# Optimization experiments

Hardware: AMD Instinct MI355X
Metric: run time of the kernel (lower is better)

The kernel has to match this reference:

```python
import jax, jax.numpy as jnp
import numpy as np

LN_EPS = 1e-5  # torch nn.LayerNorm default

def _layer_norm(x, w, b):
    m = jnp.mean(x, axis=-1, keepdims=True)
    v = jnp.mean(jnp.square(x - m), axis=-1, keepdims=True)
    return (x - m) * jax.lax.rsqrt(v + LN_EPS) * w + b

def setup_inputs() -> dict:
    R, N, D, A = 8, 8192, 2048, 128
    init_scale = 0.01
    key = jax.random.key(0)
    k0, k1, k2 = jax.random.split(key, 3)
    x = jax.random.normal(k0, (N, D), jnp.float32)
    ln_w = jnp.ones((R, D), jnp.float32)              # per-router input LayerNorm weight
    ln_b = jnp.zeros((R, D), jnp.float32)
    router_weights = jax.random.normal(k1, (R, D, A), jnp.float32) * init_scale
    rw_ln_w = jax.random.normal(k2, (R, D), jnp.float32) * init_scale  # weight-LN gamma (init ones*scale in src)
    rw_ln_b = jnp.zeros((R, D), jnp.float32)
    router_bias = jnp.zeros((R, A), jnp.float32)
    return {"x": x, "ln_w": ln_w, "ln_b": ln_b, "router_weights": router_weights,
            "rw_ln_w": rw_ln_w, "rw_ln_b": rw_ln_b, "router_bias": router_bias}

def reference(x, ln_w, ln_b, router_weights, rw_ln_w, rw_ln_b, router_bias):
    # Per-router LayerNorm of shared input x: new_x [R, N, D]
    new_x = jax.vmap(lambda w, b: _layer_norm(x, w, b))(ln_w, ln_b)
    # normalize_router_weights=True: LayerNorm over in_dim of W[i].T, then transpose back
    rw_norm = jax.vmap(lambda W, w, b: _layer_norm(W.T, w, b).T)(router_weights, rw_ln_w, rw_ln_b)  # [R, D, A]
    adapter_logits = jnp.einsum('rnd,rda->rna', new_x, rw_norm) + router_bias[:, None, :]
    adapter_probs = jax.nn.softmax(adapter_logits, axis=-1)
    return new_x, adapter_logits, adapter_probs
```

## Files before the change

### kernel.cpp

```cpp
#include <hip/hip_runtime.h>
#include <hip/hip_bf16.h>
#include <stdint.h>

#define R_ 8
#define N_ 8192
#define D_ 2048
#define A_ 128
#define J_ 1024
#define LN_EPS 1e-5f

typedef __attribute__((ext_vector_type(8))) short bf16x8;
typedef __attribute__((ext_vector_type(4))) float f32x4;

__device__ inline ushort f2bf(float f) {
    union { float f; uint32_t u; } v; v.f = f;
    uint32_t u = v.u;
    return (ushort)((u + 0x7fffu + ((u >> 16) & 1u)) >> 16);
}
__device__ inline float bf2f(ushort u) {
    union { uint32_t u; float f; } v; v.u = ((uint32_t)u) << 16;
    return v.f;
}

__global__ __launch_bounds__(256) void k_prep(
    const float* __restrict__ x,
    const float* __restrict__ W,
    const float* __restrict__ ln_w,
    const float* __restrict__ ln_b,
    const float* __restrict__ rw_w,
    const float* __restrict__ rw_b,
    const float* __restrict__ rbias,
    ushort* __restrict__ xhat,
    ushort* __restrict__ Bt,
    float* __restrict__ cvec)
{
    __shared__ float sm[16];
    const int t = threadIdx.x;

    if (blockIdx.x < N_) {
        const int n = blockIdx.x;
        const float* xr = x + (size_t)n * D_;
        float4 v0 = *(const float4*)(xr + t * 4);
        float4 v1 = *(const float4*)(xr + 1024 + t * 4);
        float s  = v0.x + v0.y + v0.z + v0.w + v1.x + v1.y + v1.z + v1.w;
        float sq = v0.x*v0.x + v0.y*v0.y + v0.z*v0.z + v0.w*v0.w
                 + v1.x*v1.x + v1.y*v1.y + v1.z*v1.z + v1.w*v1.w;
        #pragma unroll
        for (int o = 32; o > 0; o >>= 1) {
            s  += __shfl_xor(s,  o, 64);
            sq += __shfl_xor(sq, o, 64);
        }
        if ((t & 63) == 0) { sm[t >> 6] = s; sm[8 + (t >> 6)] = sq; }
        __syncthreads();
        s  = sm[0] + sm[1] + sm[2] + sm[3];
        sq = sm[8] + sm[9] + sm[10] + sm[11];
        const float mean = s * (1.0f / D_);
        const float var  = sq * (1.0f / D_) - mean * mean;
        const float rstd = rsqrtf(var + LN_EPS);

        ushort4 p0 = make_ushort4(f2bf((v0.x - mean) * rstd), f2bf((v0.y - mean) * rstd),
                                  f2bf((v0.z - mean) * rstd), f2bf((v0.w - mean) * rstd));
        ushort4 p1 = make_ushort4(f2bf((v1.x - mean) * rstd), f2bf((v1.y - mean) * rstd),
                                  f2bf((v1.z - mean) * rstd), f2bf((v1.w - mean) * rstd));
        *(ushort4*)(xhat + (size_t)n * D_ + t * 4)        = p0;
        *(ushort4*)(xhat + (size_t)n * D_ + 1024 + t * 4) = p1;
    } else {
        const int j = blockIdx.x - N_;
        const int r = j >> 7, a = j & 127;
        const float* Wc = W + (size_t)r * D_ * A_ + a;

        float vals[8];
        float s = 0.f, sq = 0.f;
        #pragma unroll
        for (int k = 0; k < 8; ++k) {
            float v = Wc[(size_t)(t + k * 256) * A_];
            vals[k] = v; s += v; sq += v * v;
        }
        #pragma unroll
        for (int o = 32; o > 0; o >>= 1) {
            s  += __shfl_xor(s,  o, 64);
            sq += __shfl_xor(sq, o, 64);
        }
        if ((t & 63) == 0) { sm[t >> 6] = s; sm[8 + (t >> 6)] = sq; }
        __syncthreads();
        s  = sm[0] + sm[1] + sm[2] + sm[3];
        sq = sm[8] + sm[9] + sm[10] + sm[11];
        const float mean = s * (1.0f / D_);
        const float var  = sq * (1.0f / D_) - mean * mean;
        const float rstd = rsqrtf(var + LN_EPS);

        float cp = 0.f;
        #pragma unroll
        for (int k = 0; k < 8; ++k) {
            const int d = t + k * 256;
            const float nv = (vals[k] - mean) * rstd * rw_w[(size_t)r * D_ + d]
                           + rw_b[(size_t)r * D_ + d];
            Bt[(size_t)j * D_ + d] = f2bf(ln_w[(size_t)r * D_ + d] * nv);
            cp += ln_b[(size_t)r * D_ + d] * nv;
        }
        __syncthreads();
        #pragma unroll
        for (int o = 32; o > 0; o >>= 1) cp += __shfl_xor(cp, o, 64);
        if ((t & 63) == 0) sm[t >> 6] = cp;
        __syncthreads();
        if (t == 0) cvec[j] = sm[0] + sm[1] + sm[2] + sm[3] + rbias[(size_t)r * A_ + a];
    }
}

__global__ __launch_bounds__(256) void k_fused(
    const ushort* __restrict__ Xh,
    const ushort* __restrict__ Bt,
    const float* __restrict__ cvec,
    const float* __restrict__ ln_w,
    const float* __restrict__ ln_b,
    float* __restrict__ new_x,
    float* __restrict__ logits,
    float* __restrict__ probs)
{
    __shared__ __attribute__((aligned(16))) ushort As[64 * 64];
    __shared__ __attribute__((aligned(16))) ushort Bs[128 * 64];
    __shared__ __attribute__((aligned(16))) ushort lwS[D_];
    __shared__ __attribute__((aligned(16))) ushort lbS[D_];

    const int t    = threadIdx.x;
    const int lane = t & 63;
    const int w    = t >> 6;
    const int r    = blockIdx.x & 7;
    const int mt   = blockIdx.x >> 3;
    const int m0   = mt * 64;
    const int j0   = r * 128;

    {
        const float4 wa = ((const float4*)(ln_w + (size_t)r * D_))[2 * t];
        const float4 wb = ((const float4*)(ln_w + (size_t)r * D_))[2 * t + 1];
        const float4 ba = ((const float4*)(ln_b + (size_t)r * D_))[2 * t];
        const float4 bb = ((const float4*)(ln_b + (size_t)r * D_))[2 * t + 1];
        *(ushort4*)(&lwS[t * 8])     = make_ushort4(f2bf(wa.x), f2bf(wa.y), f2bf(wa.z), f2bf(wa.w));
        *(ushort4*)(&lwS[t * 8 + 4]) = make_ushort4(f2bf(wb.x), f2bf(wb.y), f2bf(wb.z), f2bf(wb.w));
        *(ushort4*)(&lbS[t * 8])     = make_ushort4(f2bf(ba.x), f2bf(ba.y), f2bf(ba.z), f2bf(ba.w));
        *(ushort4*)(&lbS[t * 8 + 4]) = make_ushort4(f2bf(bb.x), f2bf(bb.y), f2bf(bb.z), f2bf(bb.w));
    }

    f32x4 acc[8];
    #pragma unroll
    for (int jf = 0; jf < 8; ++jf) acc[jf] = (f32x4){0.f, 0.f, 0.f, 0.f};

    float* nx_base = new_x + ((size_t)r * N_ + m0) * D_;

    for (int kt = 0; kt < 32; ++kt) {
        __syncthreads();
        #pragma unroll
        for (int c = 0; c < 2; ++c) {
            const int q    = t + c * 256;
            const int row  = q >> 3;
            const int slot = q & 7;
            const int kc   = slot ^ (row & 7);
            const ushort* gA = Xh + (size_t)(m0 + row) * D_ + kt * 64 + kc * 8;
            __builtin_amdgcn_global_load_lds(
                (const __attribute__((address_space(1))) void*)gA,
                (__attribute__((address_space(3))) void*)(&As[q * 8]), 16, 0, 0);
        }
        #pragma unroll
        for (int c = 0; c < 4; ++c) {
            const int q    = t + c * 256;
            const int row  = q >> 3;
            const int slot = q & 7;
            const int kc   = slot ^ (row & 7);
            const ushort* gB = Bt + (size_t)(j0 + row) * D_ + kt * 64 + kc * 8;
            __builtin_amdgcn_global_load_lds(
                (const __attribute__((address_space(1))) void*)gB,
                (__attribute__((address_space(3))) void*)(&Bs[q * 8]), 16, 0, 0);
        }
        __syncthreads();

        const int kbase = kt * 64;
        #pragma unroll
        for (int c = 0; c < 4; ++c) {
            const int q     = t + c * 256;
            const int row   = q >> 4;
            const int c4    = q & 15;
            const int pslot = (c4 >> 1) ^ (row & 7);
            const ushort4 hb = *(const ushort4*)(&As[row * 64 + pslot * 8 + (c4 & 1) * 4]);
            const int d = kbase + c4 * 4;
            const ushort4 w4 = *(const ushort4*)(&lwS[d]);
            const ushort4 b4 = *(const ushort4*)(&lbS[d]);
            f32x4 o;
            o[0] = bf2f(hb.x) * bf2f(w4.x) + bf2f(b4.x);
            o[1] = bf2f(hb.y) * bf2f(w4.y) + bf2f(b4.y);
            o[2] = bf2f(hb.z) * bf2f(w4.z) + bf2f(b4.z);
            o[3] = bf2f(hb.w) * bf2f(w4.w) + bf2f(b4.w);
            __builtin_nontemporal_store(o, (f32x4*)(nx_base + (size_t)row * D_ + d));
        }

        #pragma unroll
        for (int kf = 0; kf < 2; ++kf) {
            const int slot  = (lane >> 4) + 4 * kf;
            const int pslot = slot ^ (lane & 7);
            const bf16x8 afr = *(const bf16x8*)(&As[(w * 16 + (lane & 15)) * 64
                                                    + pslot * 8]);
            #pragma unroll
            for (int jf = 0; jf < 8; ++jf) {
                const bf16x8 bfr = *(const bf16x8*)(&Bs[(jf * 16 + (lane & 15)) * 64
                                                        + pslot * 8]);
                acc[jf] = __builtin_amdgcn_mfma_f32_16x16x32_bf16(afr, bfr, acc[jf], 0, 0, 0);
            }
        }
    }

    float cv[8];
    #pragma unroll
    for (int jf = 0; jf < 8; ++jf) cv[jf] = cvec[j0 + jf * 16 + (lane & 15)];

    #pragma unroll
    for (int reg = 0; reg < 4; ++reg) {
        const int row = m0 + w * 16 + (lane >> 4) * 4 + reg;
        float v[8], e[8];
        float mx = -3.4e38f;
        #pragma unroll
        for (int jf = 0; jf < 8; ++jf) {
            v[jf] = acc[jf][reg] + cv[jf];
            mx = fmaxf(mx, v[jf]);
        }
        #pragma unroll
        for (int o = 8; o > 0; o >>= 1) mx = fmaxf(mx, __shfl_xor(mx, o, 64));
        float ssum = 0.f;
        #pragma unroll
        for (int jf = 0; jf < 8; ++jf) { e[jf] = __expf(v[jf] - mx); ssum += e[jf]; }
        #pragma unroll
        for (int o = 8; o > 0; o >>= 1) ssum += __shfl_xor(ssum, o, 64);
        const float inv = 1.0f / ssum;
        float* lrow = logits + ((size_t)r * N_ + row) * A_;
        float* prow = probs  + ((size_t)r * N_ + row) * A_;
        #pragma unroll
        for (int jf = 0; jf < 8; ++jf) {
            const int aa = jf * 16 + (lane & 15);
            __builtin_nontemporal_store(v[jf], lrow + aa);
            __builtin_nontemporal_store(e[jf] * inv, prow + aa);
        }
    }
}

extern "C" void kernel_launch(void* const* d_in, const int* in_sizes, int n_in,
                              void* d_out, int out_size, void* d_ws, size_t ws_size,
                              hipStream_t stream)
{
    const float* x     = (const float*)d_in[0];
    const float* ln_w  = (const float*)d_in[1];
    const float* ln_b  = (const float*)d_in[2];
    const float* W     = (const float*)d_in[3];
    const float* rw_w  = (const float*)d_in[4];
    const float* rw_b  = (const float*)d_in[5];
    const float* rbias = (const float*)d_in[6];

    float* out    = (float*)d_out;
    float* new_x  = out;
    float* logits = out + (size_t)R_ * N_ * D_;
    float* probs  = logits + (size_t)R_ * N_ * A_;

    ushort* xhat = (ushort*)d_ws;
    ushort* Btp  = (ushort*)((char*)d_ws + (size_t)N_ * D_ * 2);
    float*  cvec = (float*)((char*)d_ws + (size_t)N_ * D_ * 2 + (size_t)J_ * D_ * 2);

    hipLaunchKernelGGL(k_prep, dim3(N_ + J_), dim3(256), 0, stream,
                       x, W, ln_w, ln_b, rw_w, rw_b, rbias, xhat, Btp, cvec);
    hipLaunchKernelGGL(k_fused, dim3(J_), dim3(256), 0, stream,
                       xhat, Btp, cvec, ln_w, ln_b, new_x, logits, probs);
}
```

Before: 182.8 us.

## Write new_x per full row from global X with fp32 LN params in registers

The new_x epilogue no longer reads the staged 64-column A tile from LDS. Each iteration, every half-wave group now loads a full 2048-wide row of the bf16 normalized input straight from global memory and writes whole contiguous rows of new_x, using the fp32 LayerNorm weight and bias held in registers. This removes the LDS copies of the weight and bias along with their bf16 rounding. It aims for longer contiguous output writes and less LDS traffic, at the cost of extra global reads of Xh (which may hit in cache) and more register pressure.

```diff
diff --git a/kernel.cpp b/kernel.cpp
--- a/kernel.cpp
+++ b/kernel.cpp
@@ -119,8 +119,6 @@
 {
     __shared__ __attribute__((aligned(16))) ushort As[64 * 64];
     __shared__ __attribute__((aligned(16))) ushort Bs[128 * 64];
-    __shared__ __attribute__((aligned(16))) ushort lwS[D_];
-    __shared__ __attribute__((aligned(16))) ushort lbS[D_];
 
     const int t    = threadIdx.x;
     const int lane = t & 63;
@@ -130,15 +128,12 @@
     const int m0   = mt * 64;
     const int j0   = r * 128;
 
-    {
-        const float4 wa = ((const float4*)(ln_w + (size_t)r * D_))[2 * t];
-        const float4 wb = ((const float4*)(ln_w + (size_t)r * D_))[2 * t + 1];
-        const float4 ba = ((const float4*)(ln_b + (size_t)r * D_))[2 * t];
-        const float4 bb = ((const float4*)(ln_b + (size_t)r * D_))[2 * t + 1];
-        *(ushort4*)(&lwS[t * 8])     = make_ushort4(f2bf(wa.x), f2bf(wa.y), f2bf(wa.z), f2bf(wa.w));
-        *(ushort4*)(&lwS[t * 8 + 4]) = make_ushort4(f2bf(wb.x), f2bf(wb.y), f2bf(wb.z), f2bf(wb.w));
-        *(ushort4*)(&lbS[t * 8])     = make_ushort4(f2bf(ba.x), f2bf(ba.y), f2bf(ba.z), f2bf(ba.w));
-        *(ushort4*)(&lbS[t * 8 + 4]) = make_ushort4(f2bf(bb.x), f2bf(bb.y), f2bf(bb.z), f2bf(bb.w));
+    const int cbase = (w & 1) * 1024 + lane * 4;
+    f32x4 lwv[4], lbv[4];
+    #pragma unroll
+    for (int s = 0; s < 4; ++s) {
+        lwv[s] = *(const f32x4*)(ln_w + (size_t)r * D_ + cbase + s * 256);
+        lbv[s] = *(const f32x4*)(ln_b + (size_t)r * D_ + cbase + s * 256);
     }
 
     f32x4 acc[8];
@@ -171,25 +166,26 @@
                 (const __attribute__((address_space(1))) void*)gB,
                 (__attribute__((address_space(3))) void*)(&Bs[q * 8]), 16, 0, 0);
         }
-        __syncthreads();
-
-        const int kbase = kt * 64;
-        #pragma unroll
-        for (int c = 0; c < 4; ++c) {
-            const int q     = t + c * 256;
-            const int row   = q >> 4;
-            const int c4    = q & 15;
-            const int pslot = (c4 >> 1) ^ (row & 7);
-            const ushort4 hb = *(const ushort4*)(&As[row * 64 + pslot * 8 + (c4 & 1) * 4]);
-            const int d = kbase + c4 * 4;
-            const ushort4 w4 = *(const ushort4*)(&lwS[d]);
-            const ushort4 b4 = *(const ushort4*)(&lbS[d]);
-            f32x4 o;
-            o[0] = bf2f(hb.x) * bf2f(w4.x) + bf2f(b4.x);
-            o[1] = bf2f(hb.y) * bf2f(w4.y) + bf2f(b4.y);
-            o[2] = bf2f(hb.z) * bf2f(w4.z) + bf2f(b4.z);
-            o[3] = bf2f(hb.w) * bf2f(w4.w) + bf2f(b4.w);
-            __builtin_nontemporal_store(o, (f32x4*)(nx_base + (size_t)row * D_ + d));
+
+        const int wrow = 2 * kt + (w >> 1);
+        const ushort* xs = Xh + (size_t)(m0 + wrow) * D_ + cbase;
+        ushort4 hb[4];
+        #pragma unroll
+        for (int s = 0; s < 4; ++s) hb[s] = *(const ushort4*)(xs + s * 256);
+
+        __syncthreads();
+
+        {
+            float* nd = nx_base + (size_t)wrow * D_ + cbase;
+            #pragma unroll
+            for (int s = 0; s < 4; ++s) {
+                f32x4 o;
+                o[0] = bf2f(hb[s].x) * lwv[s][0] + lbv[s][0];
+                o[1] = bf2f(hb[s].y) * lwv[s][1] + lbv[s][1];
+                o[2] = bf2f(hb[s].z) * lwv[s][2] + lbv[s][2];
+                o[3] = bf2f(hb[s].w) * lwv[s][3] + lbv[s][3];
+                __builtin_nontemporal_store(o, (f32x4*)(nd + s * 256));
+            }
         }
 
         #pragma unroll
```

Result: slower. 210.3 us (+15.0%).

## Stage softmax outputs through LDS for vectorized stores; interleave prep blocks

Applied to the files above, without the earlier changes.

The epilogue of the main kernel now writes logits and probabilities into shared memory (reusing the A/B tiles) and then writes them out as 16-byte vector nontemporal stores per thread. Previously each lane issued scalar 4-byte stores. The prep kernel also interleaves row-LayerNorm blocks with weight-column-normalization blocks (8:1) so the strided weight work is spread across the grid instead of sitting at the tail. Both changes add extra __syncthreads per output register group, and the prep grid mapping assumes the block count equals 9*1024.

```diff
diff --git a/kernel.cpp b/kernel.cpp
--- a/kernel.cpp
+++ b/kernel.cpp
@@ -36,9 +36,11 @@
 {
     __shared__ float sm[16];
     const int t = threadIdx.x;
-
-    if (blockIdx.x < N_) {
-        const int n = blockIdx.x;
+    const int g = blockIdx.x / 9;
+    const int i = blockIdx.x % 9;
+
+    if (i < 8) {
+        const int n = g * 8 + i;
         const float* xr = x + (size_t)n * D_;
         float4 v0 = *(const float4*)(xr + t * 4);
         float4 v1 = *(const float4*)(xr + 1024 + t * 4);
@@ -65,7 +67,7 @@
         *(ushort4*)(xhat + (size_t)n * D_ + t * 4)        = p0;
         *(ushort4*)(xhat + (size_t)n * D_ + 1024 + t * 4) = p1;
     } else {
-        const int j = blockIdx.x - N_;
+        const int j = g;
         const int r = j >> 7, a = j & 127;
         const float* Wc = W + (size_t)r * D_ * A_ + a;
 
@@ -207,13 +209,19 @@
         }
     }
 
+    __syncthreads();
+    float* Lv = (float*)As;
+    float* Lp = (float*)Bs;
+
     float cv[8];
     #pragma unroll
     for (int jf = 0; jf < 8; ++jf) cv[jf] = cvec[j0 + jf * 16 + (lane & 15)];
 
+    const int oidx = t >> 4;
+    const int ocg  = t & 15;
+
     #pragma unroll
     for (int reg = 0; reg < 4; ++reg) {
-        const int row = m0 + w * 16 + (lane >> 4) * 4 + reg;
         float v[8], e[8];
         float mx = -3.4e38f;
         #pragma unroll
@@ -229,14 +237,28 @@
         #pragma unroll
         for (int o = 8; o > 0; o >>= 1) ssum += __shfl_xor(ssum, o, 64);
         const float inv = 1.0f / ssum;
-        float* lrow = logits + ((size_t)r * N_ + row) * A_;
-        float* prow = probs  + ((size_t)r * N_ + row) * A_;
+
+        const int lidx = w * 4 + (lane >> 4);
         #pragma unroll
         for (int jf = 0; jf < 8; ++jf) {
-            const int aa = jf * 16 + (lane & 15);
-            __builtin_nontemporal_store(v[jf], lrow + aa);
-            __builtin_nontemporal_store(e[jf] * inv, prow + aa);
-        }
+            Lv[lidx * 128 + jf * 16 + (lane & 15)] = v[jf];
+            Lp[lidx * 128 + jf * 16 + (lane & 15)] = e[jf] * inv;
+        }
+        __syncthreads();
+        {
+            const int grow = m0 + (oidx >> 2) * 16 + (oidx & 3) * 4 + reg;
+            const f32x4 a0 = *(const f32x4*)(&Lv[oidx * 128 + ocg * 8]);
+            const f32x4 a1 = *(const f32x4*)(&Lv[oidx * 128 + ocg * 8 + 4]);
+            const f32x4 b0 = *(const f32x4*)(&Lp[oidx * 128 + ocg * 8]);
+            const f32x4 b1 = *(const f32x4*)(&Lp[oidx * 128 + ocg * 8 + 4]);
+            float* lrow = logits + ((size_t)r * N_ + grow) * A_ + ocg * 8;
+            float* prow = probs  + ((size_t)r * N_ + grow) * A_ + ocg * 8;
+            __builtin_nontemporal_store(a0, (f32x4*)lrow);
+            __builtin_nontemporal_store(a1, (f32x4*)(lrow + 4));
+            __builtin_nontemporal_store(b0, (f32x4*)prow);
+            __builtin_nontemporal_store(b1, (f32x4*)(prow + 4));
+        }
+        __syncthreads();
     }
 }
 
```

Measured after the change: 186.8 us. +2.2%, slower.
